# Performance work log

Hardware: AMD Instinct MI355X
Metric: run time of the kernel (lower is better)

The kernel has to match this reference:

```python
import jax, jax.numpy as jnp
import numpy as np

N = 100000   # nodes
E = 3200000  # edges
M = 4096     # moves
K = 16       # orders per move
NEG_SLOPE = 0.2  # PyG GATv2Conv default negative_slope

PARAM_SHAPES = {
    'g1_Wl': (10, 15), 'g1_Wr': (10, 15), 'g1_att': (10,), 'g1_b': (10,),
    'g2_Wl': (10, 25), 'g2_Wr': (10, 25), 'g2_att': (10,), 'g2_b': (10,),
    'g3_Wl': (10, 25), 'g3_Wr': (10, 25), 'g3_att': (10,), 'g3_b': (10,),
    'vt_W': (20, 29), 'vt_b': (20,), 'va_W': (1, 20), 'va_b': (1,),
    'vv_W': (10, 20), 'vv_b': (10,), 'vl_W': (1, 10), 'vl_b': (1,),
    'at_W': (20, 48), 'at_b': (20,), 'dt_W': (20, 23), 'dt_b': (20,),
    'oa_W': (1, 20), 'oa_b': (1,), 'ov_W': (1, 20), 'ov_b': (1,),
}
PARAM_NAMES = list(PARAM_SHAPES.keys())


def _linear(x, W, b):
    return x @ W.T + b


def _gatv2(x, src, dst, Wl, Wr, att, b):
    # GATv2Conv (heads=1, self-loops appended by caller), eval mode (no dropout)
    xl = x @ Wl.T  # messages from source nodes
    xr = x @ Wr.T
    e = (jax.nn.leaky_relu(xl[src] + xr[dst], NEG_SLOPE) * att).sum(-1)  # [E+N]
    emax = jax.ops.segment_max(e, dst, num_segments=N)
    ee = jnp.exp(e - emax[dst])
    denom = jax.ops.segment_sum(ee, dst, num_segments=N)
    alpha = ee / denom[dst]
    return jax.ops.segment_sum(alpha[:, None] * xl[src], dst, num_segments=N) + b


def _forward(x1, x2, edges, move_src, move_dst, move_armies, is_attack, params):
    (g1_Wl, g1_Wr, g1_att, g1_b,
     g2_Wl, g2_Wr, g2_att, g2_b,
     g3_Wl, g3_Wr, g3_att, g3_b,
     vt_W, vt_b, va_W, va_b, vv_W, vv_b, vl_W, vl_b,
     at_W, at_b, dt_W, dt_b, oa_W, oa_b, ov_W, ov_b) = params
    x2t = jnp.tile(x2, (N, 1))  # [N,4]
    self_idx = jnp.arange(N, dtype=edges.dtype)
    src = jnp.concatenate([edges[0], self_idx])
    dst = jnp.concatenate([edges[1], self_idx])
    x = jax.nn.relu(_gatv2(x1, src, dst, g1_Wl, g1_Wr, g1_att, g1_b))
    x = jax.nn.relu(_gatv2(jnp.concatenate([x, x1], 1), src, dst, g2_Wl, g2_Wr, g2_att, g2_b))
    x = jax.nn.relu(_gatv2(jnp.concatenate([x, x1], 1), src, dst, g3_Wl, g3_Wr, g3_att, g3_b))  # [N,10]
    # per-move order tensors (vectorized over [M,K]); deploy uses move_src as target
    xs, xd = x[move_src], x[move_dst]       # [M,K,10]
    x1s, x1d = x1[move_src], x1[move_dst]   # [M,K,15]
    extra = 0.6 * move_armies - 0.7 * (x1d[..., 3] + x1d[..., 4])
    attack_in = jnp.concatenate([xs, xd, x1s[..., 3:], x1d[..., 1:],
                                 move_armies[..., None], extra[..., None]], -1)  # [M,K,48]
    deploy_in = jnp.concatenate([xs, x1s[..., 3:], move_armies[..., None]], -1)  # [M,K,23]
    feat = jnp.where(is_attack[..., None] == 1,
                     _linear(attack_in, at_W, at_b),
                     _linear(deploy_in, dt_W, dt_b))
    feat = jax.nn.relu(feat)  # dropout = identity (eval)
    attn = jax.nn.softmax(_linear(feat, oa_W, oa_b), axis=1)  # softmax over orders
    p = (attn * _linear(feat, ov_W, ov_b)).sum(axis=(1, 2))   # [M]
    # value head: attention pooling over all nodes
    Vn = jax.nn.relu(_linear(jnp.concatenate([x, x1, x2t], 1), vt_W, vt_b))  # [N,20]
    vatt = jax.nn.softmax(_linear(Vn, va_W, va_b), axis=0)
    Vp = jax.nn.relu((vatt * _linear(Vn, vv_W, vv_b)).sum(axis=0))
    V = jnp.tanh(_linear(Vp, vl_W, vl_b))[0]
    return V, jax.nn.log_softmax(p, axis=0)


def setup_inputs() -> dict:
    key = jax.random.key(0)
    ks = iter(jax.random.split(key, 64))
    inp = {
        'x1': jax.random.normal(next(ks), (N, 15), jnp.float32),
        'x2': jax.random.normal(next(ks), (4,), jnp.float32),
        'edges': jax.random.randint(next(ks), (2, E), 0, N, jnp.int32),
        'move_src': jax.random.randint(next(ks), (M, K), 0, N, jnp.int32),
        'move_dst': jax.random.randint(next(ks), (M, K), 0, N, jnp.int32),
        'move_armies': jax.random.uniform(next(ks), (M, K), jnp.float32) * 10.0,
        'is_attack': jax.random.randint(next(ks), (M, K), 0, 2, jnp.int32),
    }
    for name, shape in PARAM_SHAPES.items():
        inp[name] = jax.random.normal(next(ks), shape, jnp.float32) * 0.1
    return inp


def reference(x1, x2, edges, move_src, move_dst, move_armies, is_attack,
              g1_Wl, g1_Wr, g1_att, g1_b, g2_Wl, g2_Wr, g2_att, g2_b,
              g3_Wl, g3_Wr, g3_att, g3_b, vt_W, vt_b, va_W, va_b,
              vv_W, vv_b, vl_W, vl_b, at_W, at_b, dt_W, dt_b,
              oa_W, oa_b, ov_W, ov_b):
    params = (g1_Wl, g1_Wr, g1_att, g1_b, g2_Wl, g2_Wr, g2_att, g2_b,
              g3_Wl, g3_Wr, g3_att, g3_b, vt_W, vt_b, va_W, va_b,
              vv_W, vv_b, vl_W, vl_b, at_W, at_b, dt_W, dt_b,
              oa_W, oa_b, ov_W, ov_b)
    return _forward(x1, x2, edges, move_src, move_dst, move_armies, is_attack, params)
```

## Files before the change

kernel.cpp:

```cpp
#include <hip/hip_runtime.h>
#include <hip/hip_bf16.h>
#include <hip/hip_fp16.h>
#include <math.h>

#define NN 100000
#define NE 3200000
#define MM 4096
#define KK 16
#define NEG_SLOPE 0.2f
#define SUB 8
#define BSH 8
#define NB 391
#define PCH 4096
#define FCAP 9728
#define XS 12
#define XSH 16

__device__ __forceinline__ void h10_to_f(const uint4& w0, unsigned w2, float* xs) {
    float2 f;
    f = __half22float2(*(const __half2*)&w0.x); xs[0]=f.x; xs[1]=f.y;
    f = __half22float2(*(const __half2*)&w0.y); xs[2]=f.x; xs[3]=f.y;
    f = __half22float2(*(const __half2*)&w0.z); xs[4]=f.x; xs[5]=f.y;
    f = __half22float2(*(const __half2*)&w0.w); xs[6]=f.x; xs[7]=f.y;
    f = __half22float2(*(const __half2*)&w2);   xs[8]=f.x; xs[9]=f.y;
}

__global__ __launch_bounds__(1024) void partition_kernel(const int* __restrict__ edges,
                                                         int* __restrict__ cnt,
                                                         unsigned* __restrict__ recs) {
    __shared__ unsigned rl[PCH];
    __shared__ unsigned srt[PCH];
    __shared__ unsigned short bb[PCH];
    __shared__ unsigned short bbs[PCH];
    __shared__ int h[NB];
    __shared__ int sc[1024];
    __shared__ int lb[NB];
    __shared__ int gb[NB];
    __shared__ int cur[NB];
    const int total = NE + NN;
    int base = blockIdx.x * PCH;
    int n = min(PCH, total - base);
    int t = threadIdx.x;
    if (t < NB) { h[t] = 0; cur[t] = 0; }
    __syncthreads();
    for (int j = t; j < n; j += 1024) {
        int i = base + j;
        int s, d;
        if (i < NE) { s = edges[i]; d = edges[NE + i]; }
        else        { s = i - NE; d = s; }
        rl[j] = ((unsigned)(d & 255) << 17) | (unsigned)s;
        int b = d >> BSH;
        bb[j] = (unsigned short)b;
        atomicAdd(&h[b], 1);
    }
    __syncthreads();
    int hv = (t < NB) ? h[t] : 0;
    sc[t] = hv;
    __syncthreads();
    for (int off = 1; off < 1024; off <<= 1) {
        int v = (t >= off) ? sc[t - off] : 0;
        __syncthreads();
        sc[t] += v;
        __syncthreads();
    }
    if (t < NB) {
        lb[t] = sc[t] - hv;
        if (hv > 0) gb[t] = atomicAdd(&cnt[t], hv);
    }
    __syncthreads();
    for (int j = t; j < n; j += 1024) {
        int b = bb[j];
        int l = atomicAdd(&cur[b], 1);
        int dst = lb[b] + l;
        srt[dst] = rl[j];
        bbs[dst] = (unsigned short)b;
    }
    __syncthreads();
    for (int j = t; j < n; j += 1024) {
        int b = bbs[j];
        int pos = gb[b] + (j - lb[b]);
        if (pos < FCAP) recs[(long)b * FCAP + pos] = srt[j];
    }
}

__global__ void bucket_scan_kernel(const int* __restrict__ cnt, int* __restrict__ bbase) {
    __shared__ int part[512];
    int t = threadIdx.x;
    int c = (t < NB) ? min(cnt[t], FCAP) : 0;
    part[t] = c;
    __syncthreads();
    for (int off = 1; off < 512; off <<= 1) {
        int v = (t >= off) ? part[t - off] : 0;
        __syncthreads();
        part[t] += v;
        __syncthreads();
    }
    if (t < NB) bbase[t] = part[t] - c;
    if (t == NB - 1) bbase[NB] = part[t];
}

__global__ __launch_bounds__(1024) void fine_sort_kernel(const unsigned* __restrict__ recs,
                                                         const int* __restrict__ cnt,
                                                         const int* __restrict__ bbase,
                                                         int* __restrict__ csr_src,
                                                         int* __restrict__ offsets) {
    __shared__ unsigned rl[FCAP];
    __shared__ int hist[256];
    __shared__ int sc[256];
    __shared__ int hb[257];
    __shared__ int cur[256];
    int b = blockIdx.x;
    int beg = bbase[b];
    int nb = min(cnt[b], FCAP);
    int t = threadIdx.x;
    int nodebase = b << BSH;
    int nnodes = min(256, NN - nodebase);
    if (t < 256) { hist[t] = 0; cur[t] = 0; }
    __syncthreads();
    const unsigned* rsrc = recs + (long)b * FCAP;
    for (int j = t; j < nb; j += 1024) {
        unsigned r = rsrc[j];
        rl[j] = r;
        atomicAdd(&hist[r >> 17], 1);
    }
    __syncthreads();
    int hv = (t < 256) ? hist[t] : 0;
    if (t < 256) sc[t] = hv;
    __syncthreads();
    for (int off = 1; off < 256; off <<= 1) {
        int v = 0;
        if (t < 256 && t >= off) v = sc[t - off];
        __syncthreads();
        if (t < 256) sc[t] += v;
        __syncthreads();
    }
    if (t < 256) hb[t] = sc[t] - hv;
    if (t == 0) hb[256] = nb;
    __syncthreads();
    for (int j = t; j < nb; j += 1024) {
        unsigned r = rl[j];
        int l = r >> 17;
        int p = hb[l] + atomicAdd(&cur[l], 1);
        csr_src[beg + p] = (int)(r & 0x1FFFFu);
    }
    if (t < nnodes) offsets[nodebase + t] = beg + hb[t];
    if (b == NB - 1 && t == 0) offsets[NN] = beg + nb;
}

__global__ void linear1_kernel(const float* __restrict__ x1,
                               const float* __restrict__ Wl,
                               const float* __restrict__ Wr,
                               __half* __restrict__ xlh,
                               float* __restrict__ xr) {
    int i = blockIdx.x * blockDim.x + threadIdx.x;
    if (i >= NN) return;
    float in[15];
    #pragma unroll
    for (int j = 0; j < 15; j++) in[j] = x1[i * 15 + j];
    float sl[10];
    #pragma unroll
    for (int o = 0; o < 10; o++) {
        float l = 0.f, r = 0.f;
        #pragma unroll
        for (int j = 0; j < 15; j++) {
            l += Wl[o * 15 + j] * in[j];
            r += Wr[o * 15 + j] * in[j];
        }
        sl[o] = l;
        xr[(long)i * XS + o] = r;
    }
    unsigned u[5];
    #pragma unroll
    for (int q = 0; q < 5; q++) {
        __half2 hh = __floats2half2_rn(sl[2*q], sl[2*q+1]);
        u[q] = *(unsigned*)&hh;
    }
    uint4* p4 = (uint4*)(xlh + (long)i * XSH);
    p4[0] = make_uint4(u[0], u[1], u[2], u[3]);
    *(uint2*)(xlh + (long)i * XSH + 8) = make_uint2(u[4], 0u);
}

template<bool FUSE_NEXT>
__global__ void gat_aggregate_kernel(const int* __restrict__ csr_src,
                                     const int* __restrict__ offsets,
                                     const __half* __restrict__ xlh,
                                     const float* __restrict__ xr,
                                     const float* __restrict__ att,
                                     const float* __restrict__ b,
                                     const float* __restrict__ x1,
                                     const float* __restrict__ nWl,
                                     const float* __restrict__ nWr,
                                     __half* __restrict__ xlo,
                                     float* __restrict__ xro,
                                     float* __restrict__ xout)
{
    int t = blockIdx.x * blockDim.x + threadIdx.x;
    int node = t / SUB;
    int lane = t % SUB;
    if (node >= NN) return;
    float xrn[12], a[10];
    const float4* xr4 = (const float4*)(xr + (long)node * XS);
    #pragma unroll
    for (int q = 0; q < 3; q++) {
        float4 v = xr4[q];
        xrn[4*q] = v.x; xrn[4*q+1] = v.y; xrn[4*q+2] = v.z; xrn[4*q+3] = v.w;
    }
    #pragma unroll
    for (int h = 0; h < 10; h++) a[h] = att[h];
    int beg = offsets[node], end = offsets[node + 1];
    float den = 0.f, num[10];
    #pragma unroll
    for (int h = 0; h < 10; h++) num[h] = 0.f;
    int j = beg + lane;
    for (; j + 3 * SUB < end; j += 4 * SUB) {
        int s0 = csr_src[j];
        int s1 = csr_src[j + SUB];
        int s2 = csr_src[j + 2 * SUB];
        int s3 = csr_src[j + 3 * SUB];
        const __half *p0 = xlh + (long)s0 * XSH, *p1 = xlh + (long)s1 * XSH;
        const __half *p2 = xlh + (long)s2 * XSH, *p3 = xlh + (long)s3 * XSH;
        uint4 w0a = *(const uint4*)p0; unsigned w0b = *(const unsigned*)(p0 + 8);
        uint4 w1a = *(const uint4*)p1; unsigned w1b = *(const unsigned*)(p1 + 8);
        uint4 w2a = *(const uint4*)p2; unsigned w2b = *(const unsigned*)(p2 + 8);
        uint4 w3a = *(const uint4*)p3; unsigned w3b = *(const unsigned*)(p3 + 8);
        uint4 wa[4] = {w0a, w1a, w2a, w3a};
        unsigned wb[4] = {w0b, w1b, w2b, w3b};
        #pragma unroll
        for (int q = 0; q < 4; q++) {
            float xs[10];
            h10_to_f(wa[q], wb[q], xs);
            float e = 0.f;
            #pragma unroll
            for (int h = 0; h < 10; h++) {
                float v = xs[h] + xrn[h];
                v = (v >= 0.f) ? v : NEG_SLOPE * v;
                e += v * a[h];
            }
            float w = __expf(e);
            den += w;
            #pragma unroll
            for (int h = 0; h < 10; h++) num[h] += w * xs[h];
        }
    }
    for (; j < end; j += SUB) {
        int s = csr_src[j];
        const __half* ph = xlh + (long)s * XSH;
        uint4 wa = *(const uint4*)ph;
        unsigned wb = *(const unsigned*)(ph + 8);
        float xs[10];
        h10_to_f(wa, wb, xs);
        float e = 0.f;
        #pragma unroll
        for (int h = 0; h < 10; h++) {
            float v = xs[h] + xrn[h];
            v = (v >= 0.f) ? v : NEG_SLOPE * v;
            e += v * a[h];
        }
        float w = __expf(e);
        den += w;
        #pragma unroll
        for (int h = 0; h < 10; h++) num[h] += w * xs[h];
    }
    #pragma unroll
    for (int off = SUB / 2; off; off >>= 1) {
        den += __shfl_xor(den, off, SUB);
        #pragma unroll
        for (int h = 0; h < 10; h++) num[h] += __shfl_xor(num[h], off, SUB);
    }
    float inv = 1.f / den;
    float xo[10];
    #pragma unroll
    for (int h = 0; h < 10; h++) xo[h] = fmaxf(num[h] * inv + b[h], 0.f);
    if (FUSE_NEXT) {
        if (lane < 5) {
            float in2[25];
            #pragma unroll
            for (int h = 0; h < 10; h++) in2[h] = xo[h];
            #pragma unroll
            for (int h = 0; h < 15; h++) in2[10 + h] = x1[(long)node * 15 + h];
            int o0 = 2 * lane, o1 = 2 * lane + 1;
            float sl0 = 0.f, sl1 = 0.f, sr0 = 0.f, sr1 = 0.f;
            #pragma unroll
            for (int jj = 0; jj < 25; jj++) {
                sl0 += nWl[o0 * 25 + jj] * in2[jj];
                sl1 += nWl[o1 * 25 + jj] * in2[jj];
                sr0 += nWr[o0 * 25 + jj] * in2[jj];
                sr1 += nWr[o1 * 25 + jj] * in2[jj];
            }
            __half2 hp = __floats2half2_rn(sl0, sl1);
            *(unsigned*)(xlo + (long)node * XSH + o0) = *(unsigned*)&hp;
            *(float2*)(xro + (long)node * XS + o0) = make_float2(sr0, sr1);
        }
    } else {
        if (lane == 0) {
            #pragma unroll
            for (int h = 0; h < 10; h++) xout[(long)node * XS + h] = xo[h];
        }
    }
}

__global__ void move_kernel(const float* __restrict__ x,
                            const float* __restrict__ x1,
                            const int* __restrict__ msrc,
                            const int* __restrict__ mdst,
                            const float* __restrict__ armies,
                            const int* __restrict__ isatk,
                            const float* __restrict__ at_W, const float* __restrict__ at_b,
                            const float* __restrict__ dt_W, const float* __restrict__ dt_b,
                            const float* __restrict__ oa_W, const float* __restrict__ oa_b,
                            const float* __restrict__ ov_W, const float* __restrict__ ov_b,
                            float* __restrict__ p) {
    int t = blockIdx.x * blockDim.x + threadIdx.x;
    int m = t >> 4;
    int k = t & 15;
    int s = msrc[t], d = mdst[t];
    float arm = armies[t];
    bool atk = (isatk[t] == 1);
    float xsrc[12];
    const float4* xs4 = (const float4*)(x + (long)s * XS);
    #pragma unroll
    for (int q = 0; q < 3; q++) {
        float4 v = xs4[q];
        xsrc[4*q] = v.x; xsrc[4*q+1] = v.y; xsrc[4*q+2] = v.z; xsrc[4*q+3] = v.w;
    }
    float feat[20];
    if (atk) {
        float in[48];
        #pragma unroll
        for (int h = 0; h < 10; h++) in[h] = xsrc[h];
        const float4* xd4 = (const float4*)(x + (long)d * XS);
        float xdst[12];
        #pragma unroll
        for (int q = 0; q < 3; q++) {
            float4 v = xd4[q];
            xdst[4*q] = v.x; xdst[4*q+1] = v.y; xdst[4*q+2] = v.z; xdst[4*q+3] = v.w;
        }
        #pragma unroll
        for (int h = 0; h < 10; h++) in[10 + h] = xdst[h];
        #pragma unroll
        for (int h = 0; h < 12; h++) in[20 + h] = x1[(long)s * 15 + 3 + h];
        #pragma unroll
        for (int h = 0; h < 14; h++) in[32 + h] = x1[(long)d * 15 + 1 + h];
        in[46] = arm;
        in[47] = 0.6f * arm - 0.7f * (x1[(long)d * 15 + 3] + x1[(long)d * 15 + 4]);
        #pragma unroll
        for (int o = 0; o < 20; o++) {
            float sum = at_b[o];
            #pragma unroll
            for (int j = 0; j < 48; j++) sum += at_W[o * 48 + j] * in[j];
            feat[o] = fmaxf(sum, 0.f);
        }
    } else {
        float in[23];
        #pragma unroll
        for (int h = 0; h < 10; h++) in[h] = xsrc[h];
        #pragma unroll
        for (int h = 0; h < 12; h++) in[10 + h] = x1[(long)s * 15 + 3 + h];
        in[22] = arm;
        #pragma unroll
        for (int o = 0; o < 20; o++) {
            float sum = dt_b[o];
            #pragma unroll
            for (int j = 0; j < 23; j++) sum += dt_W[o * 23 + j] * in[j];
            feat[o] = fmaxf(sum, 0.f);
        }
    }
    float oa = oa_b[0], ov = ov_b[0];
    #pragma unroll
    for (int j = 0; j < 20; j++) {
        oa += oa_W[j] * feat[j];
        ov += ov_W[j] * feat[j];
    }
    float mx = oa;
    #pragma unroll
    for (int off = 8; off; off >>= 1) mx = fmaxf(mx, __shfl_xor(mx, off, 16));
    float w = __expf(oa - mx);
    float nume = w * ov;
    float den = w;
    #pragma unroll
    for (int off = 8; off; off >>= 1) {
        nume += __shfl_xor(nume, off, 16);
        den  += __shfl_xor(den,  off, 16);
    }
    if (k == 0) p[m] = nume / den;
}

__global__ void logsoftmax_kernel(const float* __restrict__ p, float* __restrict__ out) {
    __shared__ float sm[256];
    int tid = threadIdx.x;
    float mx = -INFINITY;
    for (int i = tid; i < MM; i += 256) mx = fmaxf(mx, p[i]);
    sm[tid] = mx; __syncthreads();
    for (int s = 128; s; s >>= 1) { if (tid < s) sm[tid] = fmaxf(sm[tid], sm[tid + s]); __syncthreads(); }
    mx = sm[0]; __syncthreads();
    float sum = 0.f;
    for (int i = tid; i < MM; i += 256) sum += expf(p[i] - mx);
    sm[tid] = sum; __syncthreads();
    for (int s = 128; s; s >>= 1) { if (tid < s) sm[tid] += sm[tid + s]; __syncthreads(); }
    float ls = mx + logf(sm[0]);
    for (int i = tid; i < MM; i += 256) out[i] = p[i] - ls;
}

__global__ void value12_kernel(const float* __restrict__ x,
                               const float* __restrict__ x1,
                               const float* __restrict__ x2,
                               const float* __restrict__ vt_W, const float* __restrict__ vt_b,
                               const float* __restrict__ va_W, const float* __restrict__ va_b,
                               const float* __restrict__ vv_W, const float* __restrict__ vv_b,
                               float* __restrict__ partials) {
    __shared__ float sm[4][11];
    int i = blockIdx.x * blockDim.x + threadIdx.x;
    float w = 0.f;
    float acc[10];
    #pragma unroll
    for (int h = 0; h < 10; h++) acc[h] = 0.f;
    if (i < NN) {
        float in[29];
        const float4* xi4 = (const float4*)(x + (long)i * XS);
        float xi[12];
        #pragma unroll
        for (int q = 0; q < 3; q++) {
            float4 v = xi4[q];
            xi[4*q] = v.x; xi[4*q+1] = v.y; xi[4*q+2] = v.z; xi[4*q+3] = v.w;
        }
        #pragma unroll
        for (int h = 0; h < 10; h++) in[h] = xi[h];
        #pragma unroll
        for (int h = 0; h < 15; h++) in[10 + h] = x1[(long)i * 15 + h];
        #pragma unroll
        for (int h = 0; h < 4; h++) in[25 + h] = x2[h];
        float Vn[20];
        #pragma unroll
        for (int o = 0; o < 20; o++) {
            float s = vt_b[o];
            #pragma unroll
            for (int j = 0; j < 29; j++) s += vt_W[o * 29 + j] * in[j];
            Vn[o] = fmaxf(s, 0.f);
        }
        float lg = va_b[0];
        #pragma unroll
        for (int j = 0; j < 20; j++) lg += va_W[j] * Vn[j];
        w = __expf(lg);
        #pragma unroll
        for (int o = 0; o < 10; o++) {
            float s = vv_b[o];
            #pragma unroll
            for (int j = 0; j < 20; j++) s += vv_W[o * 20 + j] * Vn[j];
            acc[o] = w * s;
        }
    }
    #pragma unroll
    for (int off = 32; off; off >>= 1) {
        w += __shfl_xor(w, off, 64);
        #pragma unroll
        for (int h = 0; h < 10; h++) acc[h] += __shfl_xor(acc[h], off, 64);
    }
    int wid = threadIdx.x >> 6;
    if ((threadIdx.x & 63) == 0) {
        #pragma unroll
        for (int h = 0; h < 10; h++) sm[wid][h] = acc[h];
        sm[wid][10] = w;
    }
    __syncthreads();
    if (threadIdx.x < 11) {
        int c = threadIdx.x;
        partials[(long)blockIdx.x * 12 + c] = sm[0][c] + sm[1][c] + sm[2][c] + sm[3][c];
    }
}

__global__ void value3_kernel(const float* __restrict__ partials, int nparts,
                              const float* __restrict__ vl_W, const float* __restrict__ vl_b,
                              float* __restrict__ out0) {
    int lane = threadIdx.x;
    float s[11];
    #pragma unroll
    for (int c = 0; c < 11; c++) s[c] = 0.f;
    for (int j = lane; j < nparts; j += 64)
        #pragma unroll
        for (int c = 0; c < 11; c++) s[c] += partials[(long)j * 12 + c];
    #pragma unroll
    for (int off = 32; off; off >>= 1)
        #pragma unroll
        for (int c = 0; c < 11; c++) s[c] += __shfl_xor(s[c], off, 64);
    if (lane == 0) {
        float inv = 1.0f / s[10];
        float v = vl_b[0];
        #pragma unroll
        for (int h = 0; h < 10; h++) v += vl_W[h] * fmaxf(s[h] * inv, 0.f);
        out0[0] = tanhf(v);
    }
}

extern "C" void kernel_launch(void* const* d_in, const int* in_sizes, int n_in,
                              void* d_out, int out_size, void* d_ws, size_t ws_size,
                              hipStream_t stream) {
    const float* x1      = (const float*)d_in[0];
    const float* x2      = (const float*)d_in[1];
    const int*   edges   = (const int*)d_in[2];
    const int*   msrc    = (const int*)d_in[3];
    const int*   mdst    = (const int*)d_in[4];
    const float* armies  = (const float*)d_in[5];
    const int*   isatk   = (const int*)d_in[6];
    const float* g1_Wl = (const float*)d_in[7],  *g1_Wr = (const float*)d_in[8];
    const float* g1_att= (const float*)d_in[9],  *g1_b  = (const float*)d_in[10];
    const float* g2_Wl = (const float*)d_in[11], *g2_Wr = (const float*)d_in[12];
    const float* g2_att= (const float*)d_in[13], *g2_b  = (const float*)d_in[14];
    const float* g3_Wl = (const float*)d_in[15], *g3_Wr = (const float*)d_in[16];
    const float* g3_att= (const float*)d_in[17], *g3_b  = (const float*)d_in[18];
    const float* vt_W  = (const float*)d_in[19], *vt_b  = (const float*)d_in[20];
    const float* va_W  = (const float*)d_in[21], *va_b  = (const float*)d_in[22];
    const float* vv_W  = (const float*)d_in[23], *vv_b  = (const float*)d_in[24];
    const float* vl_W  = (const float*)d_in[25], *vl_b  = (const float*)d_in[26];
    const float* at_W  = (const float*)d_in[27], *at_b  = (const float*)d_in[28];
    const float* dt_W  = (const float*)d_in[29], *dt_b  = (const float*)d_in[30];
    const float* oa_W  = (const float*)d_in[31], *oa_b  = (const float*)d_in[32];
    const float* ov_W  = (const float*)d_in[33], *ov_b  = (const float*)d_in[34];

    float* out = (float*)d_out;

    float* ws = (float*)d_ws;
    __half* xlhA = (__half*)ws;
    __half* xlhB = xlhA + (long)NN * XSH;
    float* xrA = (float*)(xlhB + (long)NN * XSH);
    float* xrB = xrA + (long)NN * XS;
    float* xF  = xrB + (long)NN * XS;
    int* csr_src = (int*)(xF + (long)NN * XS);
    int* offsets = csr_src + (NE + NN);
    unsigned* recs = (unsigned*)(offsets + NN + 4);
    int* cnt   = (int*)(recs + (long)NB * FCAP);
    int* bbase = cnt + NB + 1;
    float* pbuf = (float*)(bbase + NB + 3);
    float* partials = pbuf + MM;

    const int nodeBlocks = (NN + 255) / 256;
    const int aggBlocks  = ((long)NN * SUB + 255) / 256;
    const int partBlocks = (NE + NN + PCH - 1) / PCH;

    hipMemsetAsync(cnt, 0, NB * sizeof(int), stream);
    partition_kernel<<<partBlocks, 1024, 0, stream>>>(edges, cnt, recs);
    bucket_scan_kernel<<<1, 512, 0, stream>>>(cnt, bbase);
    fine_sort_kernel<<<NB, 1024, 0, stream>>>(recs, cnt, bbase, csr_src, offsets);

    linear1_kernel<<<nodeBlocks, 256, 0, stream>>>(x1, g1_Wl, g1_Wr, xlhA, xrA);
    gat_aggregate_kernel<true><<<aggBlocks, 256, 0, stream>>>(
        csr_src, offsets, xlhA, xrA, g1_att, g1_b, x1, g2_Wl, g2_Wr, xlhB, xrB, nullptr);
    gat_aggregate_kernel<true><<<aggBlocks, 256, 0, stream>>>(
        csr_src, offsets, xlhB, xrB, g2_att, g2_b, x1, g3_Wl, g3_Wr, xlhA, xrA, nullptr);
    gat_aggregate_kernel<false><<<aggBlocks, 256, 0, stream>>>(
        csr_src, offsets, xlhA, xrA, g3_att, g3_b, x1, nullptr, nullptr, nullptr, nullptr, xF);

    move_kernel<<<(MM * KK) / 256, 256, 0, stream>>>(
        xF, x1, msrc, mdst, armies, isatk,
        at_W, at_b, dt_W, dt_b, oa_W, oa_b, ov_W, ov_b, pbuf);
    logsoftmax_kernel<<<1, 256, 0, stream>>>(pbuf, out + 1);

    value12_kernel<<<nodeBlocks, 256, 0, stream>>>(
        xF, x1, x2, vt_W, vt_b, va_W, va_b, vv_W, vv_b, partials);
    value3_kernel<<<1, 64, 0, stream>>>(partials, nodeBlocks, vl_W, vl_b, out);
}
```

Measured before the change: 377.7 us.

## Merge independent small kernels to cut launch count

New measurement: 354.9 us. -6.0%, faster.

```diff
diff --git a/kernel.cpp b/kernel.cpp
--- a/kernel.cpp
+++ b/kernel.cpp
@@ -1,5 +1,4 @@
 #include <hip/hip_runtime.h>
-#include <hip/hip_bf16.h>
 #include <hip/hip_fp16.h>
 #include <math.h>
 
@@ -15,6 +14,10 @@
 #define FCAP 9728
 #define XS 12
 #define XSH 16
+#define PART_BLOCKS ((NE + NN + PCH - 1) / PCH)
+#define LIN_BLOCKS  ((NN + 1023) / 1024)
+#define MOVE_BLOCKS ((MM * KK) / 256)
+#define VAL_BLOCKS  ((NN + 255) / 256)
 
 __device__ __forceinline__ void h10_to_f(const uint4& w0, unsigned w2, float* xs) {
     float2 f;
@@ -25,9 +28,44 @@
     f = __half22float2(*(const __half2*)&w2);   xs[8]=f.x; xs[9]=f.y;
 }
 
-__global__ __launch_bounds__(1024) void partition_kernel(const int* __restrict__ edges,
+__global__ __launch_bounds__(1024) void part_lin1_kernel(const int* __restrict__ edges,
                                                          int* __restrict__ cnt,
-                                                         unsigned* __restrict__ recs) {
+                                                         unsigned* __restrict__ recs,
+                                                         const float* __restrict__ x1,
+                                                         const float* __restrict__ Wl,
+                                                         const float* __restrict__ Wr,
+                                                         __half* __restrict__ xlh,
+                                                         float* __restrict__ xr) {
+    int t = threadIdx.x;
+    if (blockIdx.x >= PART_BLOCKS) {
+        int i = (blockIdx.x - PART_BLOCKS) * 1024 + t;
+        if (i >= NN) return;
+        float in[15];
+        #pragma unroll
+        for (int j = 0; j < 15; j++) in[j] = x1[(long)i * 15 + j];
+        float sl[10];
+        #pragma unroll
+        for (int o = 0; o < 10; o++) {
+            float l = 0.f, r = 0.f;
+            #pragma unroll
+            for (int j = 0; j < 15; j++) {
+                l += Wl[o * 15 + j] * in[j];
+                r += Wr[o * 15 + j] * in[j];
+            }
+            sl[o] = l;
+            xr[(long)i * XS + o] = r;
+        }
+        unsigned u[5];
+        #pragma unroll
+        for (int q = 0; q < 5; q++) {
+            __half2 hh = __floats2half2_rn(sl[2*q], sl[2*q+1]);
+            u[q] = *(unsigned*)&hh;
+        }
+        uint4* p4 = (uint4*)(xlh + (long)i * XSH);
+        p4[0] = make_uint4(u[0], u[1], u[2], u[3]);
+        *(uint2*)(xlh + (long)i * XSH + 8) = make_uint2(u[4], 0u);
+        return;
+    }
     __shared__ unsigned rl[PCH];
     __shared__ unsigned srt[PCH];
     __shared__ unsigned short bb[PCH];
@@ -40,7 +78,6 @@
     const int total = NE + NN;
     int base = blockIdx.x * PCH;
     int n = min(PCH, total - base);
-    int t = threadIdx.x;
     if (t < NB) { h[t] = 0; cur[t] = 0; }
     __syncthreads();
     for (int j = t; j < n; j += 1024) {
@@ -83,36 +120,33 @@
     }
 }
 
-__global__ void bucket_scan_kernel(const int* __restrict__ cnt, int* __restrict__ bbase) {
-    __shared__ int part[512];
-    int t = threadIdx.x;
-    int c = (t < NB) ? min(cnt[t], FCAP) : 0;
-    part[t] = c;
-    __syncthreads();
-    for (int off = 1; off < 512; off <<= 1) {
-        int v = (t >= off) ? part[t - off] : 0;
-        __syncthreads();
-        part[t] += v;
-        __syncthreads();
-    }
-    if (t < NB) bbase[t] = part[t] - c;
-    if (t == NB - 1) bbase[NB] = part[t];
-}
-
 __global__ __launch_bounds__(1024) void fine_sort_kernel(const unsigned* __restrict__ recs,
                                                          const int* __restrict__ cnt,
-                                                         const int* __restrict__ bbase,
                                                          int* __restrict__ csr_src,
                                                          int* __restrict__ offsets) {
     __shared__ unsigned rl[FCAP];
+    __shared__ int scn[512];
     __shared__ int hist[256];
     __shared__ int sc[256];
     __shared__ int hb[257];
     __shared__ int cur[256];
     int b = blockIdx.x;
-    int beg = bbase[b];
+    int t = threadIdx.x;
+    int c = 0;
+    if (t < 512) {
+        c = (t < NB) ? min(cnt[t], FCAP) : 0;
+        scn[t] = c;
+    }
+    __syncthreads();
+    for (int off = 1; off < 512; off <<= 1) {
+        int v = 0;
+        if (t < 512 && t >= off) v = scn[t - off];
+        __syncthreads();
+        if (t < 512) scn[t] += v;
+        __syncthreads();
+    }
+    int beg = (b == 0) ? 0 : scn[b - 1];
     int nb = min(cnt[b], FCAP);
-    int t = threadIdx.x;
     int nodebase = b << BSH;
     int nnodes = min(256, NN - nodebase);
     if (t < 256) { hist[t] = 0; cur[t] = 0; }
@@ -145,39 +179,6 @@
     }
     if (t < nnodes) offsets[nodebase + t] = beg + hb[t];
     if (b == NB - 1 && t == 0) offsets[NN] = beg + nb;
-}
-
-__global__ void linear1_kernel(const float* __restrict__ x1,
-                               const float* __restrict__ Wl,
-                               const float* __restrict__ Wr,
-                               __half* __restrict__ xlh,
-                               float* __restrict__ xr) {
-    int i = blockIdx.x * blockDim.x + threadIdx.x;
-    if (i >= NN) return;
-    float in[15];
-    #pragma unroll
-    for (int j = 0; j < 15; j++) in[j] = x1[i * 15 + j];
-    float sl[10];
-    #pragma unroll
-    for (int o = 0; o < 10; o++) {
-        float l = 0.f, r = 0.f;
-        #pragma unroll
-        for (int j = 0; j < 15; j++) {
-            l += Wl[o * 15 + j] * in[j];
-            r += Wr[o * 15 + j] * in[j];
-        }
-        sl[o] = l;
-        xr[(long)i * XS + o] = r;
-    }
-    unsigned u[5];
-    #pragma unroll
-    for (int q = 0; q < 5; q++) {
-        __half2 hh = __floats2half2_rn(sl[2*q], sl[2*q+1]);
-        u[q] = *(unsigned*)&hh;
-    }
-    uint4* p4 = (uint4*)(xlh + (long)i * XSH);
-    p4[0] = make_uint4(u[0], u[1], u[2], u[3]);
-    *(uint2*)(xlh + (long)i * XSH + 8) = make_uint2(u[4], 0u);
 }
 
 template<bool FUSE_NEXT>
@@ -299,117 +300,101 @@
     }
 }
 
-__global__ void move_kernel(const float* __restrict__ x,
-                            const float* __restrict__ x1,
-                            const int* __restrict__ msrc,
-                            const int* __restrict__ mdst,
-                            const float* __restrict__ armies,
-                            const int* __restrict__ isatk,
-                            const float* __restrict__ at_W, const float* __restrict__ at_b,
-                            const float* __restrict__ dt_W, const float* __restrict__ dt_b,
-                            const float* __restrict__ oa_W, const float* __restrict__ oa_b,
-                            const float* __restrict__ ov_W, const float* __restrict__ ov_b,
-                            float* __restrict__ p) {
-    int t = blockIdx.x * blockDim.x + threadIdx.x;
-    int m = t >> 4;
-    int k = t & 15;
-    int s = msrc[t], d = mdst[t];
-    float arm = armies[t];
-    bool atk = (isatk[t] == 1);
-    float xsrc[12];
-    const float4* xs4 = (const float4*)(x + (long)s * XS);
-    #pragma unroll
-    for (int q = 0; q < 3; q++) {
-        float4 v = xs4[q];
-        xsrc[4*q] = v.x; xsrc[4*q+1] = v.y; xsrc[4*q+2] = v.z; xsrc[4*q+3] = v.w;
-    }
-    float feat[20];
-    if (atk) {
-        float in[48];
-        #pragma unroll
-        for (int h = 0; h < 10; h++) in[h] = xsrc[h];
-        const float4* xd4 = (const float4*)(x + (long)d * XS);
-        float xdst[12];
+__global__ void move_value_kernel(const float* __restrict__ x,
+                                  const float* __restrict__ x1,
+                                  const float* __restrict__ x2,
+                                  const int* __restrict__ msrc,
+                                  const int* __restrict__ mdst,
+                                  const float* __restrict__ armies,
+                                  const int* __restrict__ isatk,
+                                  const float* __restrict__ at_W, const float* __restrict__ at_b,
+                                  const float* __restrict__ dt_W, const float* __restrict__ dt_b,
+                                  const float* __restrict__ oa_W, const float* __restrict__ oa_b,
+                                  const float* __restrict__ ov_W, const float* __restrict__ ov_b,
+                                  const float* __restrict__ vt_W, const float* __restrict__ vt_b,
+                                  const float* __restrict__ va_W, const float* __restrict__ va_b,
+                                  const float* __restrict__ vv_W, const float* __restrict__ vv_b,
+                                  float* __restrict__ p,
+                                  float* __restrict__ partials) {
+    if (blockIdx.x < MOVE_BLOCKS) {
+        int t = blockIdx.x * 256 + threadIdx.x;
+        int m = t >> 4;
+        int k = t & 15;
+        int s = msrc[t], d = mdst[t];
+        float arm = armies[t];
+        bool atk = (isatk[t] == 1);
+        float xsrc[12];
+        const float4* xs4 = (const float4*)(x + (long)s * XS);
         #pragma unroll
         for (int q = 0; q < 3; q++) {
-            float4 v = xd4[q];
-            xdst[4*q] = v.x; xdst[4*q+1] = v.y; xdst[4*q+2] = v.z; xdst[4*q+3] = v.w;
-        }
-        #pragma unroll
-        for (int h = 0; h < 10; h++) in[10 + h] = xdst[h];
-        #pragma unroll
-        for (int h = 0; h < 12; h++) in[20 + h] = x1[(long)s * 15 + 3 + h];
-        #pragma unroll
-        for (int h = 0; h < 14; h++) in[32 + h] = x1[(long)d * 15 + 1 + h];
-        in[46] = arm;
-        in[47] = 0.6f * arm - 0.7f * (x1[(long)d * 15 + 3] + x1[(long)d * 15 + 4]);
-        #pragma unroll
-        for (int o = 0; o < 20; o++) {
-            float sum = at_b[o];
-            #pragma unroll
-            for (int j = 0; j < 48; j++) sum += at_W[o * 48 + j] * in[j];
-            feat[o] = fmaxf(sum, 0.f);
-        }
-    } else {
-        float in[23];
-        #pragma unroll
-        for (int h = 0; h < 10; h++) in[h] = xsrc[h];
-        #pragma unroll
-        for (int h = 0; h < 12; h++) in[10 + h] = x1[(long)s * 15 + 3 + h];
-        in[22] = arm;
-        #pragma unroll
-        for (int o = 0; o < 20; o++) {
-            float sum = dt_b[o];
-            #pragma unroll
-            for (int j = 0; j < 23; j++) sum += dt_W[o * 23 + j] * in[j];
-            feat[o] = fmaxf(sum, 0.f);
-        }
-    }
-    float oa = oa_b[0], ov = ov_b[0];
-    #pragma unroll
-    for (int j = 0; j < 20; j++) {
-        oa += oa_W[j] * feat[j];
-        ov += ov_W[j] * feat[j];
-    }
-    float mx = oa;
-    #pragma unroll
-    for (int off = 8; off; off >>= 1) mx = fmaxf(mx, __shfl_xor(mx, off, 16));
-    float w = __expf(oa - mx);
-    float nume = w * ov;
-    float den = w;
-    #pragma unroll
-    for (int off = 8; off; off >>= 1) {
-        nume += __shfl_xor(nume, off, 16);
-        den  += __shfl_xor(den,  off, 16);
-    }
-    if (k == 0) p[m] = nume / den;
-}
-
-__global__ void logsoftmax_kernel(const float* __restrict__ p, float* __restrict__ out) {
-    __shared__ float sm[256];
-    int tid = threadIdx.x;
-    float mx = -INFINITY;
-    for (int i = tid; i < MM; i += 256) mx = fmaxf(mx, p[i]);
-    sm[tid] = mx; __syncthreads();
-    for (int s = 128; s; s >>= 1) { if (tid < s) sm[tid] = fmaxf(sm[tid], sm[tid + s]); __syncthreads(); }
-    mx = sm[0]; __syncthreads();
-    float sum = 0.f;
-    for (int i = tid; i < MM; i += 256) sum += expf(p[i] - mx);
-    sm[tid] = sum; __syncthreads();
-    for (int s = 128; s; s >>= 1) { if (tid < s) sm[tid] += sm[tid + s]; __syncthreads(); }
-    float ls = mx + logf(sm[0]);
-    for (int i = tid; i < MM; i += 256) out[i] = p[i] - ls;
-}
-
-__global__ void value12_kernel(const float* __restrict__ x,
-                               const float* __restrict__ x1,
-                               const float* __restrict__ x2,
-                               const float* __restrict__ vt_W, const float* __restrict__ vt_b,
-                               const float* __restrict__ va_W, const float* __restrict__ va_b,
-                               const float* __restrict__ vv_W, const float* __restrict__ vv_b,
-                               float* __restrict__ partials) {
+            float4 v = xs4[q];
+            xsrc[4*q]=v.x; xsrc[4*q+1]=v.y; xsrc[4*q+2]=v.z; xsrc[4*q+3]=v.w;
+        }
+        float feat[20];
+        if (atk) {
+            float in[48];
+            #pragma unroll
+            for (int h = 0; h < 10; h++) in[h] = xsrc[h];
+            const float4* xd4 = (const float4*)(x + (long)d * XS);
+            float xdst[12];
+            #pragma unroll
+            for (int q = 0; q < 3; q++) {
+                float4 v = xd4[q];
+                xdst[4*q]=v.x; xdst[4*q+1]=v.y; xdst[4*q+2]=v.z; xdst[4*q+3]=v.w;
+            }
+            #pragma unroll
+            for (int h = 0; h < 10; h++) in[10 + h] = xdst[h];
+            #pragma unroll
+            for (int h = 0; h < 12; h++) in[20 + h] = x1[(long)s * 15 + 3 + h];
+            #pragma unroll
+            for (int h = 0; h < 14; h++) in[32 + h] = x1[(long)d * 15 + 1 + h];
+            in[46] = arm;
+            in[47] = 0.6f * arm - 0.7f * (x1[(long)d * 15 + 3] + x1[(long)d * 15 + 4]);
+            #pragma unroll
+            for (int o = 0; o < 20; o++) {
+                float sum = at_b[o];
+                #pragma unroll
+                for (int j = 0; j < 48; j++) sum += at_W[o * 48 + j] * in[j];
+                feat[o] = fmaxf(sum, 0.f);
+            }
+        } else {
+            float in[23];
+            #pragma unroll
+            for (int h = 0; h < 10; h++) in[h] = xsrc[h];
+            #pragma unroll
+            for (int h = 0; h < 12; h++) in[10 + h] = x1[(long)s * 15 + 3 + h];
+            in[22] = arm;
+            #pragma unroll
+            for (int o = 0; o < 20; o++) {
+                float sum = dt_b[o];
+                #pragma unroll
+                for (int j = 0; j < 23; j++) sum += dt_W[o * 23 + j] * in[j];
+                feat[o] = fmaxf(sum, 0.f);
+            }
+        }
+        float oa = oa_b[0], ov = ov_b[0];
+        #pragma unroll
+        for (int j = 0; j < 20; j++) {
+            oa += oa_W[j] * feat[j];
+            ov += ov_W[j] * feat[j];
+        }
+        float mx = oa;
+        #pragma unroll
+        for (int off = 8; off; off >>= 1) mx = fmaxf(mx, __shfl_xor(mx, off, 16));
+        float w = __expf(oa - mx);
+        float nume = w * ov;
+        float den = w;
+        #pragma unroll
+        for (int off = 8; off; off >>= 1) {
+            nume += __shfl_xor(nume, off, 16);
+            den  += __shfl_xor(den,  off, 16);
+        }
+        if (k == 0) p[m] = nume / den;
+        return;
+    }
     __shared__ float sm[4][11];
-    int i = blockIdx.x * blockDim.x + threadIdx.x;
+    int vb = blockIdx.x - MOVE_BLOCKS;
+    int i = vb * 256 + threadIdx.x;
     float w = 0.f;
     float acc[10];
     #pragma unroll
@@ -421,7 +406,7 @@
         #pragma unroll
         for (int q = 0; q < 3; q++) {
             float4 v = xi4[q];
-            xi[4*q] = v.x; xi[4*q+1] = v.y; xi[4*q+2] = v.z; xi[4*q+3] = v.w;
+            xi[4*q]=v.x; xi[4*q+1]=v.y; xi[4*q+2]=v.z; xi[4*q+3]=v.w;
         }
         #pragma unroll
         for (int h = 0; h < 10; h++) in[h] = xi[h];
@@ -464,30 +449,47 @@
     __syncthreads();
     if (threadIdx.x < 11) {
         int c = threadIdx.x;
-        partials[(long)blockIdx.x * 12 + c] = sm[0][c] + sm[1][c] + sm[2][c] + sm[3][c];
-    }
-}
-
-__global__ void value3_kernel(const float* __restrict__ partials, int nparts,
-                              const float* __restrict__ vl_W, const float* __restrict__ vl_b,
-                              float* __restrict__ out0) {
-    int lane = threadIdx.x;
-    float s[11];
-    #pragma unroll
-    for (int c = 0; c < 11; c++) s[c] = 0.f;
-    for (int j = lane; j < nparts; j += 64)
-        #pragma unroll
-        for (int c = 0; c < 11; c++) s[c] += partials[(long)j * 12 + c];
-    #pragma unroll
-    for (int off = 32; off; off >>= 1)
-        #pragma unroll
-        for (int c = 0; c < 11; c++) s[c] += __shfl_xor(s[c], off, 64);
-    if (lane == 0) {
-        float inv = 1.0f / s[10];
-        float v = vl_b[0];
-        #pragma unroll
-        for (int h = 0; h < 10; h++) v += vl_W[h] * fmaxf(s[h] * inv, 0.f);
-        out0[0] = tanhf(v);
+        partials[(long)vb * 12 + c] = sm[0][c] + sm[1][c] + sm[2][c] + sm[3][c];
+    }
+}
+
+__global__ void final_kernel(const float* __restrict__ p,
+                             const float* __restrict__ partials,
+                             const float* __restrict__ vl_W, const float* __restrict__ vl_b,
+                             float* __restrict__ out) {
+    if (blockIdx.x == 0) {
+        __shared__ float sm[256];
+        int tid = threadIdx.x;
+        float mx = -INFINITY;
+        for (int i = tid; i < MM; i += 256) mx = fmaxf(mx, p[i]);
+        sm[tid] = mx; __syncthreads();
+        for (int s = 128; s; s >>= 1) { if (tid < s) sm[tid] = fmaxf(sm[tid], sm[tid + s]); __syncthreads(); }
+        mx = sm[0]; __syncthreads();
+        float sum = 0.f;
+        for (int i = tid; i < MM; i += 256) sum += expf(p[i] - mx);
+        sm[tid] = sum; __syncthreads();
+        for (int s = 128; s; s >>= 1) { if (tid < s) sm[tid] += sm[tid + s]; __syncthreads(); }
+        float ls = mx + logf(sm[0]);
+        for (int i = tid; i < MM; i += 256) out[1 + i] = p[i] - ls;
+    } else if (threadIdx.x < 64) {
+        int lane = threadIdx.x;
+        float s[11];
+        #pragma unroll
+        for (int c = 0; c < 11; c++) s[c] = 0.f;
+        for (int j = lane; j < VAL_BLOCKS; j += 64)
+            #pragma unroll
+            for (int c = 0; c < 11; c++) s[c] += partials[(long)j * 12 + c];
+        #pragma unroll
+        for (int off = 32; off; off >>= 1)
+            #pragma unroll
+            for (int c = 0; c < 11; c++) s[c] += __shfl_xor(s[c], off, 64);
+        if (lane == 0) {
+            float inv = 1.0f / s[10];
+            float v = vl_b[0];
+            #pragma unroll
+            for (int h = 0; h < 10; h++) v += vl_W[h] * fmaxf(s[h] * inv, 0.f);
+            out[0] = tanhf(v);
+        }
     }
 }
 
@@ -528,33 +530,24 @@
     int* offsets = csr_src + (NE + NN);
     unsigned* recs = (unsigned*)(offsets + NN + 4);
     int* cnt   = (int*)(recs + (long)NB * FCAP);
-    int* bbase = cnt + NB + 1;
-    float* pbuf = (float*)(bbase + NB + 3);
+    float* pbuf = (float*)(cnt + NB + 1);
     float* partials = pbuf + MM;
 
-    const int nodeBlocks = (NN + 255) / 256;
-    const int aggBlocks  = ((long)NN * SUB + 255) / 256;
-    const int partBlocks = (NE + NN + PCH - 1) / PCH;
+    const int aggBlocks = ((long)NN * SUB + 255) / 256;
 
     hipMemsetAsync(cnt, 0, NB * sizeof(int), stream);
-    partition_kernel<<<partBlocks, 1024, 0, stream>>>(edges, cnt, recs);
-    bucket_scan_kernel<<<1, 512, 0, stream>>>(cnt, bbase);
-    fine_sort_kernel<<<NB, 1024, 0, stream>>>(recs, cnt, bbase, csr_src, offsets);
-
-    linear1_kernel<<<nodeBlocks, 256, 0, stream>>>(x1, g1_Wl, g1_Wr, xlhA, xrA);
+    part_lin1_kernel<<<PART_BLOCKS + LIN_BLOCKS, 1024, 0, stream>>>(
+        edges, cnt, recs, x1, g1_Wl, g1_Wr, xlhA, xrA);
+    fine_sort_kernel<<<NB, 1024, 0, stream>>>(recs, cnt, csr_src, offsets);
     gat_aggregate_kernel<true><<<aggBlocks, 256, 0, stream>>>(
         csr_src, offsets, xlhA, xrA, g1_att, g1_b, x1, g2_Wl, g2_Wr, xlhB, xrB, nullptr);
     gat_aggregate_kernel<true><<<aggBlocks, 256, 0, stream>>>(
         csr_src, offsets, xlhB, xrB, g2_att, g2_b, x1, g3_Wl, g3_Wr, xlhA, xrA, nullptr);
     gat_aggregate_kernel<false><<<aggBlocks, 256, 0, stream>>>(
         csr_src, offsets, xlhA, xrA, g3_att, g3_b, x1, nullptr, nullptr, nullptr, nullptr, xF);
-
-    move_kernel<<<(MM * KK) / 256, 256, 0, stream>>>(
-        xF, x1, msrc, mdst, armies, isatk,
-        at_W, at_b, dt_W, dt_b, oa_W, oa_b, ov_W, ov_b, pbuf);
-    logsoftmax_kernel<<<1, 256, 0, stream>>>(pbuf, out + 1);
-
-    value12_kernel<<<nodeBlocks, 256, 0, stream>>>(
-        xF, x1, x2, vt_W, vt_b, va_W, va_b, vv_W, vv_b, partials);
-    value3_kernel<<<1, 64, 0, stream>>>(partials, nodeBlocks, vl_W, vl_b, out);
-}
+    move_value_kernel<<<MOVE_BLOCKS + VAL_BLOCKS, 256, 0, stream>>>(
+        xF, x1, x2, msrc, mdst, armies, isatk,
+        at_W, at_b, dt_W, dt_b, oa_W, oa_b, ov_W, ov_b,
+        vt_W, vt_b, va_W, va_b, vv_W, vv_b, pbuf, partials);
+    final_kernel<<<2, 256, 0, stream>>>(pbuf, partials, vl_W, vl_b, out);
+}
```
